# Performance work log

Hardware: AMD Instinct MI355X
Metric: run time of the kernel (lower is better)

Reference implementation:

```python
import jax, jax.numpy as jnp
import numpy as np

NH = 25            # nHidden
NS = 20            # nStep (MPC horizon)
DT = 1.0 / 60.0    # del_t
EPS = 1e-4
PQ = 5.0           # terminal cost weight
QV = 200.0         # velocity cost weight
QA = 1.0           # control cost weight
BATCH = 131072
D = NH + 2         # augmented state dim


def setup_inputs() -> dict:
    key = jax.random.key(0)
    k1, k2, k3, k4, k5 = jax.random.split(key, 5)
    x = jax.random.normal(k1, (BATCH, NH), jnp.float32)
    gripper_p = jax.random.normal(k2, (BATCH,), jnp.float32)
    gripper_v = jax.random.normal(k3, (BATCH,), jnp.float32)
    # learned parameters of the module
    Af = jax.random.uniform(k4, (NH, 1), jnp.float32)               # feature->position coupling column
    Lq = jnp.tril(jax.random.uniform(k5, (NH, NH), jnp.float32))    # Cholesky-style factor of Q0
    return {"x": x, "gripper_p": gripper_p, "gripper_v": gripper_v, "Af": Af, "Lq": Lq}


def _build_system(Af, Lq):
    """Assemble the (batch-shared) MPC matrices: Q_final, p_final, S_, T_."""
    eyeD = jnp.eye(D, dtype=Af.dtype)
    # A0 = [[I, 0, Af], [0 .. 0, [1 dt; 0 1]]]
    top = jnp.concatenate([jnp.eye(NH, dtype=Af.dtype), jnp.zeros((NH, 1), Af.dtype), Af], axis=1)
    ap = jnp.concatenate([jnp.zeros((2, NH), Af.dtype),
                          jnp.array([[1.0, DT], [0.0, 1.0]], Af.dtype)], axis=1)
    A0 = jnp.concatenate([top, ap], axis=0)                                   # [D, D]
    B0 = jnp.concatenate([jnp.zeros((NH, 1), Af.dtype),
                          jnp.array([[0.5 * DT * DT], [DT]], Af.dtype)], axis=0)  # [D, 1]
    # stage cost Q0 (padded with [0 0; 0 Qv] block)
    Q0 = Lq @ Lq.T + EPS * jnp.eye(NH, dtype=Af.dtype)
    Q0f = (jnp.zeros((D, D), Af.dtype)
           .at[:NH, :NH].set(Q0)
           .at[NH:, NH:].set(jnp.array([[0.0, 0.0], [0.0, QV]], Af.dtype)))
    # powers A0^0..A0^NS (small fixed loop, NS=20)
    pows = [eyeD]
    for _ in range(NS):
        pows.append(pows[-1] @ A0)
    P = jnp.stack(pows)                    # [NS+1, D, D]
    T_ = P[1:].reshape(NS * D, D)          # stacked A0^1..A0^NS
    # S_ block (r,c) = A0^(r-c) @ B0 for c<=r (block lower-triangular), else 0
    SB = P @ B0                            # [NS+1, D, 1]
    r = jnp.arange(NS)
    diff = r[:, None] - r[None, :]         # [NS, NS]
    Sblk = jnp.where((diff >= 0)[:, :, None, None], SB[jnp.clip(diff, 0)], 0.0)  # [NS, NS, D, 1]
    S_ = Sblk.transpose(0, 2, 1, 3).reshape(NS * D, NS)
    # block-diagonal Q (last block scaled by Pq)
    Qblocks = jnp.concatenate([jnp.tile(Q0f[None], (NS - 1, 1, 1)), PQ * Q0f[None]], axis=0)
    Qd = jnp.zeros((NS, D, NS, D), Af.dtype).at[r, :, r, :].set(Qblocks).reshape(NS * D, NS * D)
    QS = Qd @ S_                                                       # [NS*D, NS]
    Q_final = 2.0 * (QA * jnp.eye(NS, dtype=Af.dtype) + S_.T @ QS) + EPS * jnp.eye(NS, dtype=Af.dtype)
    p_final = 2.0 * (T_.T @ QS)                                        # [D, NS]
    return Q_final, p_final, S_, T_


def reference(x, gripper_p, gripper_v, Af, Lq):
    nB = x.shape[0]
    Q_final, p_final, S_, T_ = _build_system(Af, Lq)
    x0 = jnp.concatenate([x, gripper_p[:, None], gripper_v[:, None]], axis=1)  # [B, D]
    p = x0 @ p_final                                                           # [B, NS]
    # QP with G=0, h=0 (trivially satisfied) and no equality constraints ->
    # unconstrained minimizer: u = -Q_final^{-1} p
    u = -jnp.linalg.solve(Q_final, p.T).T                                      # [B, NS]
    x_predict = u @ S_.T + x0 @ T_.T                                           # [B, NS*D]
    # output selector picks the gripper position entry (index NH) of each block
    return x_predict.reshape(nB, NS, D)[:, :, NH]                              # [B, NS]
```

## Files before the change

### kernel.cpp

```cpp
#include <hip/hip_runtime.h>

#define NHID 25
#define NSTEP 20
#define DT_ (1.0/60.0)
#define EPS_ 1e-4
#define PQ_ 5.0
#define QV_ 200.0
#define QA_ 1.0

__global__ __launch_bounds__(256, 2) void mpc_fused(
    const float* __restrict__ x, const float* __restrict__ gp,
    const float* __restrict__ gv, const float* __restrict__ Af,
    const float* __restrict__ Lq, float* __restrict__ out)
{
    __shared__ float xs[256 * NHID];
    __shared__ float Lqs[NHID * NHID];
    __shared__ float us[NHID];
    __shared__ float bs[NSTEP];
    __shared__ float gs[NSTEP];

    const int t = threadIdx.x;
    const size_t b0 = (size_t)blockIdx.x * 256;

    double af = 0.0;
    if (t < NHID) af = (double)Af[t];
    for (int i = t; i < NHID * NHID; i += 256) Lqs[i] = Lq[i];
    {
        const float4* xsrc = (const float4*)(x + b0 * NHID);
        float4* xdst = (float4*)xs;
        #pragma unroll
        for (int i = 0; i < 7; ++i) {
            int idx = t + 256 * i;
            if (idx < 1600) xdst[idx] = xsrc[idx];
        }
    }
    const float p = gp[b0 + t];
    const float v = gv[b0 + t];
    __syncthreads();

    if (t < 64) {
        const double dt = DT_;
        const int tr = (t < NHID) ? t : 0;

        double wv = 0.0;
        #pragma unroll
        for (int i = 0; i < NHID; ++i) {
            double afi = __shfl(af, i, 64);
            if (i >= t && t < NHID) wv += (double)Lqs[i * NHID + tr] * afi;
        }
        double uv = EPS_ * af;
        #pragma unroll
        for (int j = 0; j < NHID; ++j) {
            double wj = __shfl(wv, j, 64);
            if (j <= t && t < NHID) uv += (double)Lqs[tr * NHID + j] * wj;
        }
        double av = af * uv;
        #pragma unroll
        for (int off = 32; off >= 1; off >>= 1)
            av += __shfl_xor(av, off, 64);
        const double alpha = av;

        double row[NSTEP + 2];
        #pragma unroll
        for (int c = 0; c < NSTEP; ++c) {
            int m0 = (t > c) ? t : c;
            double s = 0.0;
            for (int rr = m0; rr < NSTEP; ++rr) {
                double wr = (rr == NSTEP - 1) ? PQ_ : 1.0;
                s += wr * ((double)(rr - t) * (double)(rr - c) * alpha + QV_);
            }
            row[c] = 2.0 * dt * dt * s + ((t == c) ? (2.0 * QA_ + EPS_) : 0.0);
        }
        {
            double s20 = 0.0, s21 = 0.0;
            for (int rr = t; rr < NSTEP; ++rr) {
                double wr = (rr == NSTEP - 1) ? PQ_ : 1.0;
                s20 += wr * (double)(rr - t);
                s21 += wr * ((double)(rr + 1) * (double)(rr - t) * alpha + QV_);
            }
            row[NSTEP]     = s20;
            row[NSTEP + 1] = s21;
        }

        #pragma unroll
        for (int piv = 0; piv < NSTEP; ++piv) {
            double pr[NSTEP + 2];
            #pragma unroll
            for (int c = piv; c < NSTEP + 2; ++c)
                pr[c] = __shfl(row[c], piv, 64);
            double pinv = 1.0 / pr[piv];
            double f = row[piv] * pinv;
            #pragma unroll
            for (int c = piv; c < NSTEP + 2; ++c) {
                double nv = row[c] - f * pr[c];
                row[c] = (t == piv) ? (pr[c] * pinv) : nv;
            }
        }
        double z1 = row[NSTEP], z2 = row[NSTEP + 1];

        const double hdt2 = 0.5 * dt * dt;
        double bacc = 0.0, gacc = 0.0;
        #pragma unroll
        for (int c = 0; c < NSTEP; ++c) {
            double z1c = __shfl(z1, c, 64);
            double z2c = __shfl(z2, c, 64);
            if (c <= t) {
                double ssel = hdt2 + (double)(t - c) * dt * dt;
                bacc += z1c * ssel;
                gacc += z2c * ssel;
            }
        }
        if (t < NHID) us[t] = (float)uv;
        if (t < NSTEP) {
            bs[t] = (float)(-2.0 * dt * bacc);
            gs[t] = (float)((double)(t + 1) * dt - 2.0 * dt * gacc);
        }
    }
    __syncthreads();

    const float* xr = xs + t * NHID;
    float tb = 0.0f;
    #pragma unroll
    for (int i = 0; i < NHID; ++i)
        tb = fmaf(xr[i], us[i], tb);

    float4* o4 = (float4*)(out + (b0 + t) * NSTEP);
    #pragma unroll
    for (int q = 0; q < 5; ++q) {
        float4 r;
        r.x = fmaf(tb, bs[4*q+0], fmaf(v, gs[4*q+0], p));
        r.y = fmaf(tb, bs[4*q+1], fmaf(v, gs[4*q+1], p));
        r.z = fmaf(tb, bs[4*q+2], fmaf(v, gs[4*q+2], p));
        r.w = fmaf(tb, bs[4*q+3], fmaf(v, gs[4*q+3], p));
        o4[q] = r;
    }
}

extern "C" void kernel_launch(void* const* d_in, const int* in_sizes, int n_in,
                              void* d_out, int out_size, void* d_ws, size_t ws_size,
                              hipStream_t stream) {
    const float* x  = (const float*)d_in[0];
    const float* gp = (const float*)d_in[1];
    const float* gv = (const float*)d_in[2];
    const float* Af = (const float*)d_in[3];
    const float* Lq = (const float*)d_in[4];
    float* out = (float*)d_out;

    const int B = in_sizes[1];
    hipLaunchKernelGGL(mpc_fused, dim3(B / 256), dim3(256), 0, stream,
                       x, gp, gv, Af, Lq, out);
}
```

Baseline: 94.51 us.

## Split batch-shared QP setup into single-block kernel, stream main kernel

Moves the batch-independent computation (Q0-weighted coupling, 20x20 elimination in double precision, and the b/g coefficient vectors) out of every block into a one-block setup kernel that writes 65 floats to workspace. The main kernel then just loads those constants and runs the memory-bound per-row dot product and output write. This removes the redundant per-block double-precision serial solve that stalled each block before streaming. The cost is an extra kernel launch and a serial dependency between the two launches.

```diff
diff --git a/kernel.cpp b/kernel.cpp
--- a/kernel.cpp
+++ b/kernel.cpp
@@ -8,23 +8,114 @@
 #define QV_ 200.0
 #define QA_ 1.0
 
-__global__ __launch_bounds__(256, 2) void mpc_fused(
+__global__ __launch_bounds__(64) void setup_kernel(
+    const float* __restrict__ Af, const float* __restrict__ Lq,
+    float* __restrict__ C)
+{
+    __shared__ float  Afs[NHID];
+    __shared__ double wv_[NHID];
+    __shared__ double uv_[NHID];
+    __shared__ double alpha_s;
+    __shared__ double zs[2][NSTEP];
+
+    const int t = threadIdx.x;
+    const double dt = DT_;
+
+    if (t < NHID) Afs[t] = Af[t];
+    __syncthreads();
+
+    if (t < NHID) {
+        double acc = 0.0;
+        for (int i = t; i < NHID; ++i)
+            acc += (double)Lq[i * NHID + t] * (double)Afs[i];
+        wv_[t] = acc;
+    }
+    __syncthreads();
+    if (t < NHID) {
+        double acc = EPS_ * (double)Afs[t];
+        for (int j = 0; j <= t; ++j)
+            acc += (double)Lq[t * NHID + j] * wv_[j];
+        uv_[t] = acc;
+    }
+    __syncthreads();
+    if (t == 0) {
+        double a = 0.0;
+        for (int i = 0; i < NHID; ++i) a += (double)Afs[i] * uv_[i];
+        alpha_s = a;
+    }
+    __syncthreads();
+    const double alpha = alpha_s;
+
+    double row[NSTEP + 2];
+    #pragma unroll
+    for (int c = 0; c < NSTEP; ++c) {
+        int m0 = (t > c) ? t : c;
+        double s = 0.0;
+        for (int rr = m0; rr < NSTEP; ++rr) {
+            double wr = (rr == NSTEP - 1) ? PQ_ : 1.0;
+            s += wr * ((double)(rr - t) * (double)(rr - c) * alpha + QV_);
+        }
+        row[c] = 2.0 * dt * dt * s + ((t == c) ? (2.0 * QA_ + EPS_) : 0.0);
+    }
+    {
+        double s20 = 0.0, s21 = 0.0;
+        for (int rr = t; rr < NSTEP; ++rr) {
+            double wr = (rr == NSTEP - 1) ? PQ_ : 1.0;
+            s20 += wr * (double)(rr - t);
+            s21 += wr * ((double)(rr + 1) * (double)(rr - t) * alpha + QV_);
+        }
+        row[NSTEP]     = s20;
+        row[NSTEP + 1] = s21;
+    }
+
+    #pragma unroll
+    for (int piv = 0; piv < NSTEP; ++piv) {
+        double pr[NSTEP + 2];
+        #pragma unroll
+        for (int c = piv; c < NSTEP + 2; ++c)
+            pr[c] = __shfl(row[c], piv, 64);
+        __builtin_amdgcn_sched_barrier(0);
+        double pinv = 1.0 / pr[piv];
+        double f = row[piv] * pinv;
+        #pragma unroll
+        for (int c = piv; c < NSTEP + 2; ++c) {
+            double nv = row[c] - f * pr[c];
+            row[c] = (t == piv) ? (pr[c] * pinv) : nv;
+        }
+    }
+    if (t < NSTEP) { zs[0][t] = row[NSTEP]; zs[1][t] = row[NSTEP + 1]; }
+    __syncthreads();
+
+    if (t < NHID) C[t] = (float)uv_[t];
+    if (t < NSTEP) {
+        const double hdt2 = 0.5 * dt * dt;
+        double bacc = 0.0, gacc = 0.0;
+        for (int c = 0; c <= t; ++c) {
+            double ssel = hdt2 + (double)(t - c) * dt * dt;
+            bacc += zs[0][c] * ssel;
+            gacc += zs[1][c] * ssel;
+        }
+        C[32 + t] = (float)(-2.0 * dt * bacc);
+        C[64 + t] = (float)((double)(t + 1) * dt - 2.0 * dt * gacc);
+    }
+}
+
+__global__ __launch_bounds__(256) void mpc_main(
     const float* __restrict__ x, const float* __restrict__ gp,
-    const float* __restrict__ gv, const float* __restrict__ Af,
-    const float* __restrict__ Lq, float* __restrict__ out)
+    const float* __restrict__ gv, const float* __restrict__ C,
+    float* __restrict__ out)
 {
     __shared__ float xs[256 * NHID];
-    __shared__ float Lqs[NHID * NHID];
     __shared__ float us[NHID];
     __shared__ float bs[NSTEP];
     __shared__ float gs[NSTEP];
-
     const int t = threadIdx.x;
     const size_t b0 = (size_t)blockIdx.x * 256;
 
-    double af = 0.0;
-    if (t < NHID) af = (double)Af[t];
-    for (int i = t; i < NHID * NHID; i += 256) Lqs[i] = Lq[i];
+    if (t < NHID)                us[t] = C[t];
+    else if (t >= 32 && t < 52)  bs[t - 32] = C[t];
+    else if (t >= 64 && t < 84)  gs[t - 64] = C[t];
+
     {
         const float4* xsrc = (const float4*)(x + b0 * NHID);
         float4* xdst = (float4*)xs;
@@ -36,86 +127,6 @@
     }
     const float p = gp[b0 + t];
     const float v = gv[b0 + t];
-    __syncthreads();
-
-    if (t < 64) {
-        const double dt = DT_;
-        const int tr = (t < NHID) ? t : 0;
-
-        double wv = 0.0;
-        #pragma unroll
-        for (int i = 0; i < NHID; ++i) {
-            double afi = __shfl(af, i, 64);
-            if (i >= t && t < NHID) wv += (double)Lqs[i * NHID + tr] * afi;
-        }
-        double uv = EPS_ * af;
-        #pragma unroll
-        for (int j = 0; j < NHID; ++j) {
-            double wj = __shfl(wv, j, 64);
-            if (j <= t && t < NHID) uv += (double)Lqs[tr * NHID + j] * wj;
-        }
-        double av = af * uv;
-        #pragma unroll
-        for (int off = 32; off >= 1; off >>= 1)
-            av += __shfl_xor(av, off, 64);
-        const double alpha = av;
-
-        double row[NSTEP + 2];
-        #pragma unroll
-        for (int c = 0; c < NSTEP; ++c) {
-            int m0 = (t > c) ? t : c;
-            double s = 0.0;
-            for (int rr = m0; rr < NSTEP; ++rr) {
-                double wr = (rr == NSTEP - 1) ? PQ_ : 1.0;
-                s += wr * ((double)(rr - t) * (double)(rr - c) * alpha + QV_);
-            }
-            row[c] = 2.0 * dt * dt * s + ((t == c) ? (2.0 * QA_ + EPS_) : 0.0);
-        }
-        {
-            double s20 = 0.0, s21 = 0.0;
-            for (int rr = t; rr < NSTEP; ++rr) {
-                double wr = (rr == NSTEP - 1) ? PQ_ : 1.0;
-                s20 += wr * (double)(rr - t);
-                s21 += wr * ((double)(rr + 1) * (double)(rr - t) * alpha + QV_);
-            }
-            row[NSTEP]     = s20;
-            row[NSTEP + 1] = s21;
-        }
-
-        #pragma unroll
-        for (int piv = 0; piv < NSTEP; ++piv) {
-            double pr[NSTEP + 2];
-            #pragma unroll
-            for (int c = piv; c < NSTEP + 2; ++c)
-                pr[c] = __shfl(row[c], piv, 64);
-            double pinv = 1.0 / pr[piv];
-            double f = row[piv] * pinv;
-            #pragma unroll
-            for (int c = piv; c < NSTEP + 2; ++c) {
-                double nv = row[c] - f * pr[c];
-                row[c] = (t == piv) ? (pr[c] * pinv) : nv;
-            }
-        }
-        double z1 = row[NSTEP], z2 = row[NSTEP + 1];
-
-        const double hdt2 = 0.5 * dt * dt;
-        double bacc = 0.0, gacc = 0.0;
-        #pragma unroll
-        for (int c = 0; c < NSTEP; ++c) {
-            double z1c = __shfl(z1, c, 64);
-            double z2c = __shfl(z2, c, 64);
-            if (c <= t) {
-                double ssel = hdt2 + (double)(t - c) * dt * dt;
-                bacc += z1c * ssel;
-                gacc += z2c * ssel;
-            }
-        }
-        if (t < NHID) us[t] = (float)uv;
-        if (t < NSTEP) {
-            bs[t] = (float)(-2.0 * dt * bacc);
-            gs[t] = (float)((double)(t + 1) * dt - 2.0 * dt * gacc);
-        }
-    }
     __syncthreads();
 
     const float* xr = xs + t * NHID;
@@ -145,8 +156,10 @@
     const float* Af = (const float*)d_in[3];
     const float* Lq = (const float*)d_in[4];
     float* out = (float*)d_out;
+    float* C   = (float*)d_ws;
 
     const int B = in_sizes[1];
-    hipLaunchKernelGGL(mpc_fused, dim3(B / 256), dim3(256), 0, stream,
-                       x, gp, gv, Af, Lq, out);
+    hipLaunchKernelGGL(setup_kernel, dim3(1), dim3(64), 0, stream, Af, Lq, C);
+    hipLaunchKernelGGL(mpc_main, dim3(B / 256), dim3(256), 0, stream,
+                       x, gp, gv, C, out);
 }
```

Measured after the change: 95.47 us. No clear change (+1.0%).
